# Kernel tuning notes

Measured on AMD Instinct MI355X. Metric: run time of the kernel, lower is better.

The kernel has to match this reference:

```python
import jax, jax.numpy as jnp
import numpy as np

B, S, E = 2, 2048, 2048
HQ, HK, D = 32, 8, 64
G = HQ // HK  # GQA groups

def _rope(t, cos, sin):
    # t: [B,S,H,D]; cos/sin: [1,S,1,D/2]
    t1, t2 = jnp.split(t, 2, axis=-1)
    return jnp.concatenate([t1 * cos - t2 * sin, t2 * cos + t1 * sin], axis=-1)

def setup_inputs() -> dict:
    key = jax.random.key(0)
    ks = jax.random.split(key, 8)
    sc = 1.0 / np.sqrt(E)
    return {
        "x": jax.random.normal(ks[0], (B, S, E), jnp.float32),
        "rope_cos": jax.random.uniform(ks[1], (1, S, 1, D // 2), jnp.float32),
        "rope_sin": jax.random.uniform(ks[2], (1, S, 1, D // 2), jnp.float32),
        "attn_mask": jnp.zeros((1, 1, S, S), jnp.float32),
        "Wq": jax.random.normal(ks[3], (E, HQ, D), jnp.float32) * sc,
        "Wk": jax.random.normal(ks[4], (E, HK, D), jnp.float32) * sc,
        "Wv": jax.random.normal(ks[5], (E, HK, D), jnp.float32) * sc,
        "Wo": jax.random.normal(ks[6], (HQ, D, E), jnp.float32) * (1.0 / np.sqrt(HQ * D)),
    }

def reference(x, rope_cos, rope_sin, attn_mask, Wq, Wk, Wv, Wo):
    # QKV projections (LinearGeneral, no bias)
    q = jnp.einsum('bse,ehd->bshd', x, Wq)
    k = jnp.einsum('bse,ehd->bshd', x, Wk)
    v = jnp.einsum('bse,ehd->bshd', x, Wv)
    # inline RoPE on q and k
    q = _rope(q, rope_cos, rope_sin)
    k = _rope(k, rope_cos, rope_sin)
    # [B,H,S,D]
    q = jnp.transpose(q, (0, 2, 1, 3))
    k = jnp.transpose(k, (0, 2, 1, 3))
    v = jnp.transpose(v, (0, 2, 1, 3))
    # GQA repeat of k/v to full query-head count (faithful to jnp.repeat in source)
    k = jnp.repeat(k, G, axis=1)
    v = jnp.repeat(v, G, axis=1)
    # explicit scores (NOTE: source applies no 1/sqrt(d) scaling)
    w = jnp.einsum('bhqd,bhkd->bhqk', q, k) + attn_mask
    w = jax.nn.softmax(w, axis=-1)
    o = jnp.einsum('bhqk,bhkd->bhqd', w, v)
    o = jnp.transpose(o, (0, 2, 1, 3))  # [B,S,H,D]
    return jnp.einsum('bshd,hde->bse', o, Wo)
```

## Files before the change

kernel.cpp:

```cpp
#include <hip/hip_runtime.h>
#include <hip/hip_bf16.h>

typedef __bf16 bf16_t;
typedef __bf16 bfrag __attribute__((ext_vector_type(8)));
typedef float f4 __attribute__((ext_vector_type(4)));

#define S_LEN 2048
#define HQ_N 32
#define HK_N 8
#define D_DIM 64
#define LOG2E 1.4426950408889634f

__global__ __launch_bounds__(256) void cvt_bf16(
    const float* __restrict__ src, bf16_t* __restrict__ dst, int n)
{
    int i = (blockIdx.x * 256 + threadIdx.x) * 8;
    if (i >= n) return;
    f4 a = *(const f4*)(src + i);
    f4 b = *(const f4*)(src + i + 4);
    bf16_t o[8];
#pragma unroll
    for (int j = 0; j < 4; ++j) { o[j] = (bf16_t)a[j]; o[4 + j] = (bf16_t)b[j]; }
    *(uint4*)(dst + i) = *(uint4*)o;
}

__global__ __launch_bounds__(256) void transpose_cvt(
    const float* __restrict__ src, bf16_t* __restrict__ dst,
    int K, int N, int row_off)
{
    __shared__ float T[32][33];
    const int n0 = blockIdx.x * 32;
    const int k0 = blockIdx.y * 32;
    const int tx = threadIdx.x;
    const int ty = threadIdx.y;
#pragma unroll
    for (int i = 0; i < 4; ++i)
        T[ty + 8 * i][tx] = src[(size_t)(k0 + ty + 8 * i) * N + n0 + tx];
    __syncthreads();
#pragma unroll
    for (int i = 0; i < 4; ++i)
        dst[(size_t)(row_off + n0 + ty + 8 * i) * K + k0 + tx] =
            (bf16_t)T[tx][ty + 8 * i];
}

template<bool OUT_BF16>
__global__ __launch_bounds__(256) void gemm_bt(
    const bf16_t* __restrict__ A, const bf16_t* __restrict__ Bt,
    void* __restrict__ Cv, int M, int N, int K, int ldc)
{
    __shared__ bf16_t As[128][72];
    __shared__ bf16_t Bs[128][72];
    const int tid  = threadIdx.x;
    const int wave = tid >> 6;
    const int lane = tid & 63;
    const int lrow = lane & 15;
    const int quad = lane >> 4;
    const int wm   = (wave >> 1) * 64;
    const int wn   = (wave & 1) * 64;
    const int bm   = blockIdx.y * 128;
    const int bn   = blockIdx.x * 128;

    f4 acc[4][4];
#pragma unroll
    for (int i = 0; i < 4; ++i)
#pragma unroll
        for (int j = 0; j < 4; ++j)
            acc[i][j] = (f4){0.f, 0.f, 0.f, 0.f};

    const int sr = tid >> 2;
    const int sc = (tid & 3) * 16;

    for (int k0 = 0; k0 < K; k0 += 64) {
        uint4 a0 = *(const uint4*)(A  + (size_t)(bm + sr)      * K + k0 + sc);
        uint4 a1 = *(const uint4*)(A  + (size_t)(bm + sr)      * K + k0 + sc + 8);
        uint4 a2 = *(const uint4*)(A  + (size_t)(bm + sr + 64) * K + k0 + sc);
        uint4 a3 = *(const uint4*)(A  + (size_t)(bm + sr + 64) * K + k0 + sc + 8);
        uint4 b0 = *(const uint4*)(Bt + (size_t)(bn + sr)      * K + k0 + sc);
        uint4 b1 = *(const uint4*)(Bt + (size_t)(bn + sr)      * K + k0 + sc + 8);
        uint4 b2 = *(const uint4*)(Bt + (size_t)(bn + sr + 64) * K + k0 + sc);
        uint4 b3 = *(const uint4*)(Bt + (size_t)(bn + sr + 64) * K + k0 + sc + 8);
        __syncthreads();
        *(uint4*)(&As[sr][sc])          = a0;
        *(uint4*)(&As[sr][sc + 8])      = a1;
        *(uint4*)(&As[sr + 64][sc])     = a2;
        *(uint4*)(&As[sr + 64][sc + 8]) = a3;
        *(uint4*)(&Bs[sr][sc])          = b0;
        *(uint4*)(&Bs[sr][sc + 8])      = b1;
        *(uint4*)(&Bs[sr + 64][sc])     = b2;
        *(uint4*)(&Bs[sr + 64][sc + 8]) = b3;
        __syncthreads();

#pragma unroll
        for (int kc = 0; kc < 2; ++kc) {
            bfrag aF[4], bF[4];
#pragma unroll
            for (int i = 0; i < 4; ++i)
                aF[i] = *(const bfrag*)(&As[wm + i * 16 + lrow][kc * 32 + quad * 8]);
#pragma unroll
            for (int j = 0; j < 4; ++j)
                bF[j] = *(const bfrag*)(&Bs[wn + j * 16 + lrow][kc * 32 + quad * 8]);
#pragma unroll
            for (int i = 0; i < 4; ++i)
#pragma unroll
                for (int j = 0; j < 4; ++j)
                    acc[i][j] = __builtin_amdgcn_mfma_f32_16x16x32_bf16(
                        aF[i], bF[j], acc[i][j], 0, 0, 0);
        }
    }

#pragma unroll
    for (int i = 0; i < 4; ++i)
#pragma unroll
        for (int j = 0; j < 4; ++j)
#pragma unroll
            for (int r = 0; r < 4; ++r) {
                int row = bm + wm + i * 16 + quad * 4 + r;
                int col = bn + wn + j * 16 + lrow;
                if (OUT_BF16)
                    ((bf16_t*)Cv)[(size_t)row * ldc + col] = (bf16_t)acc[i][j][r];
                else
                    ((float*)Cv)[(size_t)row * ldc + col] = acc[i][j][r];
            }
}

__global__ __launch_bounds__(256) void rope_fused(
    bf16_t* __restrict__ t, const float* __restrict__ cs,
    const float* __restrict__ sn)
{
    int idx = blockIdx.x * 256 + threadIdx.x;
    int cidx = idx % 1280;
    int row  = idx / 1280;
    int s    = row & (S_LEN - 1);
    int col, d1;
    float scale;
    if (cidx < 1024) {
        d1 = cidx & 31;
        col = (cidx >> 5) * 64 + d1;
        scale = LOG2E;
    } else {
        int c2 = cidx - 1024;
        d1 = c2 & 31;
        col = 2048 + (c2 >> 5) * 64 + d1;
        scale = 1.0f;
    }
    size_t base = (size_t)row * 3072 + col;
    float t1 = (float)t[base];
    float t2 = (float)t[base + 32];
    float c  = cs[s * 32 + d1];
    float s_ = sn[s * 32 + d1];
    t[base]      = (bf16_t)((t1 * c - t2 * s_) * scale);
    t[base + 32] = (bf16_t)((t2 * c + t1 * s_) * scale);
}

__global__ __launch_bounds__(256) void attn_mfma(
    const bf16_t* __restrict__ qkv, const float* __restrict__ mask,
    bf16_t* __restrict__ o)
{
    __shared__ bf16_t Ks[64][72];
    __shared__ bf16_t Vt[64][72];
    __shared__ bf16_t Ps[128][72];

    const int tid  = threadIdx.x;
    const int wave = tid >> 6;
    const int lane = tid & 63;
    const int lrow = lane & 15;
    const int quad = lane >> 4;
    const int qt   = blockIdx.x;
    const int h    = blockIdx.y;
    const int b    = blockIdx.z;
    const int hk   = h >> 2;
    const int s0   = qt * 128;
    const int wrow = wave * 32;

    bfrag vOnes;
#pragma unroll
    for (int j = 0; j < 8; ++j) vOnes[j] = (lrow == 0) ? (bf16_t)1.0f : (bf16_t)0.0f;

    bfrag qf[2][2];
#pragma unroll
    for (int m = 0; m < 2; ++m) {
        const bf16_t* qsrc = qkv + (size_t)(b * S_LEN + s0 + wrow + m * 16 + lrow) * 3072 + h * 64;
#pragma unroll
        for (int c = 0; c < 2; ++c)
            qf[m][c] = *(const bfrag*)(qsrc + c * 32 + quad * 8);
    }

    f4 oacc[2][4], lacc[2];
#pragma unroll
    for (int m = 0; m < 2; ++m) {
        lacc[m] = (f4){0.f, 0.f, 0.f, 0.f};
#pragma unroll
        for (int n = 0; n < 4; ++n) oacc[m][n] = (f4){0.f, 0.f, 0.f, 0.f};
    }

    const int skey = tid >> 2;
    const int sdc  = (tid & 3) * 16;
    const int vg   = tid >> 5;
    const int vp   = tid & 31;

    for (int kt = 0; kt < 32; ++kt) {
        const bf16_t* ksrc = qkv + (size_t)(b * S_LEN + kt * 64 + skey) * 3072 + 2048 + hk * 64 + sdc;
        uint4 k0 = *(const uint4*)(ksrc);
        uint4 k1 = *(const uint4*)(ksrc + 8);
        unsigned int vw[8];
#pragma unroll
        for (int kk = 0; kk < 8; ++kk)
            vw[kk] = *(const unsigned int*)(qkv + (size_t)(b * S_LEN + kt * 64 + vg * 8 + kk) * 3072
                                            + 2560 + hk * 64 + 2 * vp);
        __syncthreads();
        *(uint4*)(&Ks[skey][sdc])     = k0;
        *(uint4*)(&Ks[skey][sdc + 8]) = k1;
        {
            unsigned short lo[8], hi[8];
#pragma unroll
            for (int kk = 0; kk < 8; ++kk) { lo[kk] = vw[kk] & 0xffff; hi[kk] = vw[kk] >> 16; }
            *(uint4*)(&Vt[2 * vp][vg * 8])     = *(uint4*)lo;
            *(uint4*)(&Vt[2 * vp + 1][vg * 8]) = *(uint4*)hi;
        }
        __syncthreads();

        float mk[2][4][4];
#pragma unroll
        for (int m = 0; m < 2; ++m)
#pragma unroll
            for (int n = 0; n < 4; ++n)
#pragma unroll
                for (int r = 0; r < 4; ++r)
                    mk[m][n][r] = mask[(size_t)(s0 + wrow + m * 16 + quad * 4 + r) * S_LEN
                                       + kt * 64 + n * 16 + lrow];

        bfrag kf[4][2];
#pragma unroll
        for (int n = 0; n < 4; ++n)
#pragma unroll
            for (int c = 0; c < 2; ++c)
                kf[n][c] = *(const bfrag*)(&Ks[n * 16 + lrow][c * 32 + quad * 8]);

        f4 sc[2][4];
#pragma unroll
        for (int m = 0; m < 2; ++m)
#pragma unroll
            for (int n = 0; n < 4; ++n) {
                f4 a = (f4){0.f, 0.f, 0.f, 0.f};
                a = __builtin_amdgcn_mfma_f32_16x16x32_bf16(qf[m][0], kf[n][0], a, 0, 0, 0);
                a = __builtin_amdgcn_mfma_f32_16x16x32_bf16(qf[m][1], kf[n][1], a, 0, 0, 0);
                sc[m][n] = a;
            }

#pragma unroll
        for (int m = 0; m < 2; ++m)
#pragma unroll
            for (int n = 0; n < 4; ++n)
#pragma unroll
                for (int r = 0; r < 4; ++r) {
                    float p = exp2f(fmaf(mk[m][n][r], LOG2E, sc[m][n][r]));
                    Ps[wrow + m * 16 + quad * 4 + r][n * 16 + lrow] = (bf16_t)p;
                }

        bfrag pf[2][2], vf[4][2];
#pragma unroll
        for (int m = 0; m < 2; ++m)
#pragma unroll
            for (int c = 0; c < 2; ++c)
                pf[m][c] = *(const bfrag*)(&Ps[wrow + m * 16 + lrow][c * 32 + quad * 8]);
#pragma unroll
        for (int n = 0; n < 4; ++n)
#pragma unroll
            for (int c = 0; c < 2; ++c)
                vf[n][c] = *(const bfrag*)(&Vt[n * 16 + lrow][c * 32 + quad * 8]);
#pragma unroll
        for (int m = 0; m < 2; ++m) {
#pragma unroll
            for (int n = 0; n < 4; ++n) {
                oacc[m][n] = __builtin_amdgcn_mfma_f32_16x16x32_bf16(pf[m][0], vf[n][0], oacc[m][n], 0, 0, 0);
                oacc[m][n] = __builtin_amdgcn_mfma_f32_16x16x32_bf16(pf[m][1], vf[n][1], oacc[m][n], 0, 0, 0);
            }
            lacc[m] = __builtin_amdgcn_mfma_f32_16x16x32_bf16(pf[m][0], vOnes, lacc[m], 0, 0, 0);
            lacc[m] = __builtin_amdgcn_mfma_f32_16x16x32_bf16(pf[m][1], vOnes, lacc[m], 0, 0, 0);
        }
    }

#pragma unroll
    for (int m = 0; m < 2; ++m)
#pragma unroll
        for (int r = 0; r < 4; ++r) {
            float lv = __shfl(lacc[m][r], lane & 48, 64);
            float inv = 1.f / lv;
            int row = b * S_LEN + s0 + wrow + m * 16 + quad * 4 + r;
#pragma unroll
            for (int n = 0; n < 4; ++n)
                o[(size_t)row * 2048 + h * 64 + n * 16 + lrow] = (bf16_t)(oacc[m][n][r] * inv);
        }
}

extern "C" void kernel_launch(void* const* d_in, const int* in_sizes, int n_in,
                              void* d_out, int out_size, void* d_ws, size_t ws_size,
                              hipStream_t stream)
{
    const float* x    = (const float*)d_in[0];
    const float* rc   = (const float*)d_in[1];
    const float* rs   = (const float*)d_in[2];
    const float* mask = (const float*)d_in[3];
    const float* Wq   = (const float*)d_in[4];
    const float* Wk   = (const float*)d_in[5];
    const float* Wv   = (const float*)d_in[6];
    const float* Wo   = (const float*)d_in[7];
    float* out = (float*)d_out;

    char* ws = (char*)d_ws;
    bf16_t* qkv = (bf16_t*)(ws);
    bf16_t* xb  = (bf16_t*)(ws + (24u << 20));
    bf16_t* ob  = xb;
    bf16_t* Wt3 = (bf16_t*)(ws + (40u << 20));
    bf16_t* Wot = (bf16_t*)(ws + (52u << 20));

    const int M = 2 * S_LEN;
    dim3 blk(256);

    cvt_bf16<<<(M * 2048) / (256 * 8), blk, 0, stream>>>(x, xb, M * 2048);
    transpose_cvt<<<dim3(64, 64), dim3(32, 8), 0, stream>>>(Wq, Wt3, 2048, 2048, 0);
    transpose_cvt<<<dim3(16, 64), dim3(32, 8), 0, stream>>>(Wk, Wt3, 2048,  512, 2048);
    transpose_cvt<<<dim3(16, 64), dim3(32, 8), 0, stream>>>(Wv, Wt3, 2048,  512, 2560);
    transpose_cvt<<<dim3(64, 64), dim3(32, 8), 0, stream>>>(Wo, Wot, 2048, 2048, 0);

    gemm_bt<true><<<dim3(3072 / 128, M / 128), blk, 0, stream>>>(
        xb, Wt3, qkv, M, 3072, 2048, 3072);

    rope_fused<<<(M * 1280) / 256, blk, 0, stream>>>(qkv, rc, rs);

    attn_mfma<<<dim3(16, 32, 2), blk, 0, stream>>>(qkv, mask, ob);

    gemm_bt<false><<<dim3(2048 / 128, M / 128), blk, 0, stream>>>(
        ob, Wot, out, M, 2048, 2048, 2048);
}
```

Baseline: 422.0 us.

## Pre-transpose mask and V into bf16 global buffers and fold mask into MFMA accumulator

Adds a pre-pass that transposes the fp32 attention mask into a bf16 buffer pre-scaled by log2(e), and a second pass that writes V transposed per KV head into a global buffer. The attention kernel then loads V with coalesced 16-byte vector loads and stores it straight to shared memory, with no lane-by-lane shuffling. It also seeds each score MFMA accumulator with the mask values, which removes the separate FMA before exp2. This cuts strided 4-byte V loads and fp32 mask traffic inside the hot loop, at the cost of two extra kernel launches and extra global writes. The mask buffer reuses the weight workspace region after the QKV GEMM, and storing the mask in bf16 loses precision for non-zero masks.

```diff
diff --git a/kernel.cpp b/kernel.cpp
--- a/kernel.cpp
+++ b/kernel.cpp
@@ -3,6 +3,7 @@
 
 typedef __bf16 bf16_t;
 typedef __bf16 bfrag __attribute__((ext_vector_type(8)));
+typedef __bf16 b4 __attribute__((ext_vector_type(4)));
 typedef float f4 __attribute__((ext_vector_type(4)));
 
 #define S_LEN 2048
@@ -26,7 +27,7 @@
 
 __global__ __launch_bounds__(256) void transpose_cvt(
     const float* __restrict__ src, bf16_t* __restrict__ dst,
-    int K, int N, int row_off)
+    int K, int N, int row_off, float scale)
 {
     __shared__ float T[32][33];
     const int n0 = blockIdx.x * 32;
@@ -40,7 +41,31 @@
 #pragma unroll
     for (int i = 0; i < 4; ++i)
         dst[(size_t)(row_off + n0 + ty + 8 * i) * K + k0 + tx] =
-            (bf16_t)T[tx][ty + 8 * i];
+            (bf16_t)(T[tx][ty + 8 * i] * scale);
+}
+
+__global__ __launch_bounds__(256) void transpose_v(
+    const bf16_t* __restrict__ qkv, bf16_t* __restrict__ Vtg)
+{
+    __shared__ bf16_t T[32][66];
+    const int s0 = blockIdx.x * 32;
+    const int bh = blockIdx.y;
+    const int b  = bh >> 3;
+    const int hk = bh & 7;
+    const int tx = threadIdx.x;
+    const int ty = threadIdx.y;
+#pragma unroll
+    for (int i = 0; i < 4; ++i) {
+        const bf16_t* src = qkv + (size_t)(b * S_LEN + s0 + ty + 8 * i) * 3072 + 2560 + hk * 64;
+        T[ty + 8 * i][tx]      = src[tx];
+        T[ty + 8 * i][tx + 32] = src[tx + 32];
+    }
+    __syncthreads();
+#pragma unroll
+    for (int i = 0; i < 8; ++i) {
+        int d = ty + 8 * i;
+        Vtg[(size_t)(bh * 64 + d) * S_LEN + s0 + tx] = T[tx][d];
+    }
 }
 
 template<bool OUT_BF16>
@@ -153,8 +178,8 @@
 }
 
 __global__ __launch_bounds__(256) void attn_mfma(
-    const bf16_t* __restrict__ qkv, const float* __restrict__ mask,
-    bf16_t* __restrict__ o)
+    const bf16_t* __restrict__ qkv, const bf16_t* __restrict__ Vtg,
+    const bf16_t* __restrict__ maskT, bf16_t* __restrict__ o)
 {
     __shared__ bf16_t Ks[64][72];
     __shared__ bf16_t Vt[64][72];
@@ -185,6 +210,11 @@
             qf[m][c] = *(const bfrag*)(qsrc + c * 32 + quad * 8);
     }
 
+    const bf16_t* mbase[2];
+#pragma unroll
+    for (int m = 0; m < 2; ++m)
+        mbase[m] = maskT + (size_t)lrow * S_LEN + s0 + wrow + m * 16 + quad * 4;
+
     f4 oacc[2][4], lacc[2];
 #pragma unroll
     for (int m = 0; m < 2; ++m) {
@@ -195,39 +225,21 @@
 
     const int skey = tid >> 2;
     const int sdc  = (tid & 3) * 16;
-    const int vg   = tid >> 5;
-    const int vp   = tid & 31;
+    const bf16_t* vsrc0 = Vtg + (size_t)((b * 8 + hk) * 64 + skey) * S_LEN + sdc;
 
     for (int kt = 0; kt < 32; ++kt) {
         const bf16_t* ksrc = qkv + (size_t)(b * S_LEN + kt * 64 + skey) * 3072 + 2048 + hk * 64 + sdc;
         uint4 k0 = *(const uint4*)(ksrc);
         uint4 k1 = *(const uint4*)(ksrc + 8);
-        unsigned int vw[8];
-#pragma unroll
-        for (int kk = 0; kk < 8; ++kk)
-            vw[kk] = *(const unsigned int*)(qkv + (size_t)(b * S_LEN + kt * 64 + vg * 8 + kk) * 3072
-                                            + 2560 + hk * 64 + 2 * vp);
+        const bf16_t* vsrc = vsrc0 + kt * 64;
+        uint4 v0 = *(const uint4*)(vsrc);
+        uint4 v1 = *(const uint4*)(vsrc + 8);
         __syncthreads();
         *(uint4*)(&Ks[skey][sdc])     = k0;
         *(uint4*)(&Ks[skey][sdc + 8]) = k1;
-        {
-            unsigned short lo[8], hi[8];
-#pragma unroll
-            for (int kk = 0; kk < 8; ++kk) { lo[kk] = vw[kk] & 0xffff; hi[kk] = vw[kk] >> 16; }
-            *(uint4*)(&Vt[2 * vp][vg * 8])     = *(uint4*)lo;
-            *(uint4*)(&Vt[2 * vp + 1][vg * 8]) = *(uint4*)hi;
-        }
+        *(uint4*)(&Vt[skey][sdc])     = v0;
+        *(uint4*)(&Vt[skey][sdc + 8]) = v1;
         __syncthreads();
-
-        float mk[2][4][4];
-#pragma unroll
-        for (int m = 0; m < 2; ++m)
-#pragma unroll
-            for (int n = 0; n < 4; ++n)
-#pragma unroll
-                for (int r = 0; r < 4; ++r)
-                    mk[m][n][r] = mask[(size_t)(s0 + wrow + m * 16 + quad * 4 + r) * S_LEN
-                                       + kt * 64 + n * 16 + lrow];
 
         bfrag kf[4][2];
 #pragma unroll
@@ -241,7 +253,8 @@
         for (int m = 0; m < 2; ++m)
 #pragma unroll
             for (int n = 0; n < 4; ++n) {
-                f4 a = (f4){0.f, 0.f, 0.f, 0.f};
+                b4 mv = *(const b4*)(mbase[m] + (size_t)(kt * 64 + n * 16) * S_LEN);
+                f4 a = (f4){(float)mv[0], (float)mv[1], (float)mv[2], (float)mv[3]};
                 a = __builtin_amdgcn_mfma_f32_16x16x32_bf16(qf[m][0], kf[n][0], a, 0, 0, 0);
                 a = __builtin_amdgcn_mfma_f32_16x16x32_bf16(qf[m][1], kf[n][1], a, 0, 0, 0);
                 sc[m][n] = a;
@@ -253,7 +266,7 @@
             for (int n = 0; n < 4; ++n)
 #pragma unroll
                 for (int r = 0; r < 4; ++r) {
-                    float p = exp2f(fmaf(mk[m][n][r], LOG2E, sc[m][n][r]));
+                    float p = exp2f(sc[m][n][r]);
                     Ps[wrow + m * 16 + quad * 4 + r][n * 16 + lrow] = (bf16_t)p;
                 }
 
@@ -308,27 +321,33 @@
     float* out = (float*)d_out;
 
     char* ws = (char*)d_ws;
-    bf16_t* qkv = (bf16_t*)(ws);
-    bf16_t* xb  = (bf16_t*)(ws + (24u << 20));
-    bf16_t* ob  = xb;
-    bf16_t* Wt3 = (bf16_t*)(ws + (40u << 20));
-    bf16_t* Wot = (bf16_t*)(ws + (52u << 20));
+    bf16_t* qkv   = (bf16_t*)(ws);
+    bf16_t* xb    = (bf16_t*)(ws + (24u << 20));
+    bf16_t* ob    = xb;
+    bf16_t* Wt3   = (bf16_t*)(ws + (40u << 20));
+    bf16_t* maskT = (bf16_t*)(ws + (40u << 20));
+    bf16_t* Vtg   = (bf16_t*)(ws + (48u << 20));
+    bf16_t* Wot   = (bf16_t*)(ws + (52u << 20));
 
     const int M = 2 * S_LEN;
     dim3 blk(256);
 
     cvt_bf16<<<(M * 2048) / (256 * 8), blk, 0, stream>>>(x, xb, M * 2048);
-    transpose_cvt<<<dim3(64, 64), dim3(32, 8), 0, stream>>>(Wq, Wt3, 2048, 2048, 0);
-    transpose_cvt<<<dim3(16, 64), dim3(32, 8), 0, stream>>>(Wk, Wt3, 2048,  512, 2048);
-    transpose_cvt<<<dim3(16, 64), dim3(32, 8), 0, stream>>>(Wv, Wt3, 2048,  512, 2560);
-    transpose_cvt<<<dim3(64, 64), dim3(32, 8), 0, stream>>>(Wo, Wot, 2048, 2048, 0);
+    transpose_cvt<<<dim3(64, 64), dim3(32, 8), 0, stream>>>(Wq, Wt3, 2048, 2048, 0, 1.0f);
+    transpose_cvt<<<dim3(16, 64), dim3(32, 8), 0, stream>>>(Wk, Wt3, 2048,  512, 2048, 1.0f);
+    transpose_cvt<<<dim3(16, 64), dim3(32, 8), 0, stream>>>(Wv, Wt3, 2048,  512, 2560, 1.0f);
+    transpose_cvt<<<dim3(64, 64), dim3(32, 8), 0, stream>>>(Wo, Wot, 2048, 2048, 0, 1.0f);
 
     gemm_bt<true><<<dim3(3072 / 128, M / 128), blk, 0, stream>>>(
         xb, Wt3, qkv, M, 3072, 2048, 3072);
 
     rope_fused<<<(M * 1280) / 256, blk, 0, stream>>>(qkv, rc, rs);
 
-    attn_mfma<<<dim3(16, 32, 2), blk, 0, stream>>>(qkv, mask, ob);
+    transpose_cvt<<<dim3(64, 64), dim3(32, 8), 0, stream>>>(
+        mask, maskT, S_LEN, S_LEN, 0, LOG2E);
+    transpose_v<<<dim3(64, 16), dim3(32, 8), 0, stream>>>(qkv, Vtg);
+
+    attn_mfma<<<dim3(16, 32, 2), blk, 0, stream>>>(qkv, Vtg, maskT, ob);
 
     gemm_bt<false><<<dim3(2048 / 128, M / 128), blk, 0, stream>>>(
         ob, Wot, out, M, 2048, 2048, 2048);
```

After: 435.8 us. +3.3%, slower.
